# Optimization experiments

Measured on AMD Instinct MI355X. Metric: run time of the kernel, lower is better.

The kernel has to match this reference:

```python
import jax, jax.numpy as jnp
import numpy as np

N = 100000
E = 1600000
F_IN = 64
HID = 64
OUT = 64


def _sage_conv(x, src, dst, w_l, b_l, w_r):
    # PyG SAGEConv (mean aggr): out = lin_l(mean_{j in N(i)} x_j) + lin_r(x_i)
    msgs = x[src]                                             # [E, F] gather
    summed = jax.ops.segment_sum(msgs, dst, num_segments=N)   # [N, F]
    ones = jnp.ones((src.shape[0],), dtype=x.dtype)
    cnt = jax.ops.segment_sum(ones, dst, num_segments=N)      # [N]
    mean = summed / jnp.maximum(cnt, 1.0)[:, None]
    return mean @ w_l + b_l + x @ w_r


def setup_inputs() -> dict:
    key = jax.random.key(0)
    ks = jax.random.split(key, 12)
    sc = lambda f: 1.0 / np.sqrt(f)
    inp = {
        "h": jax.random.normal(ks[0], (N, F_IN), dtype=jnp.float32),
        "edge_index": jax.random.randint(ks[1], (2, E), 0, N, dtype=jnp.int64),
        # conv1: lin_l (with bias) and lin_r (no bias), weights stored [in, out]
        "w1_l": jax.random.normal(ks[2], (F_IN, HID), dtype=jnp.float32) * sc(F_IN),
        "b1_l": jnp.zeros((HID,), dtype=jnp.float32),
        "w1_r": jax.random.normal(ks[3], (F_IN, HID), dtype=jnp.float32) * sc(F_IN),
        "w_lin1": jax.random.normal(ks[4], (HID, HID), dtype=jnp.float32) * sc(HID),
        "b_lin1": jnp.zeros((HID,), dtype=jnp.float32),
        "w2_l": jax.random.normal(ks[5], (HID, HID), dtype=jnp.float32) * sc(HID),
        "b2_l": jnp.zeros((HID,), dtype=jnp.float32),
        "w2_r": jax.random.normal(ks[6], (HID, HID), dtype=jnp.float32) * sc(HID),
        "w_lin2": jax.random.normal(ks[7], (HID, OUT), dtype=jnp.float32) * sc(HID),
        "b_lin2": jnp.zeros((OUT,), dtype=jnp.float32),
    }
    return inp


def reference(h, edge_index, w1_l, b1_l, w1_r, w_lin1, b_lin1,
              w2_l, b2_l, w2_r, w_lin2, b_lin2):
    src, dst = edge_index[0], edge_index[1]
    x = jax.nn.relu(_sage_conv(h, src, dst, w1_l, b1_l, w1_r))
    x = jax.nn.relu(x @ w_lin1 + b_lin1)
    x = jax.nn.relu(_sage_conv(x, src, dst, w2_l, b2_l, w2_r))
    x = x @ w_lin2 + b_lin2
    return x
```

## Files before the change

kernel.cpp:

```cpp
#include <hip/hip_runtime.h>
#include <hip/hip_fp16.h>

#define FEAT   64
#define BSHIFT 8
#define BNODES 256
#define MAXB   512
#define CHUNK  4096
#define REGION 5120

typedef _Float16 half8 __attribute__((ext_vector_type(8)));
typedef float  float4v __attribute__((ext_vector_type(4)));

__global__ __launch_bounds__(512) void prep_kernel(
    const int* __restrict__ esrc, const int* __restrict__ edst,
    int* __restrict__ bcur, int* __restrict__ pedge, int E, int PB,
    const float* __restrict__ h, __half* __restrict__ h16,
    int n4, int CVB,
    const float* w0, const float* w1, const float* w2,
    const float* w3, const float* w4, const float* w5,
    __half* __restrict__ wT)
{
    __shared__ int cnt[MAXB];
    __shared__ int sa[MAXB], sb[MAXB];
    __shared__ int gb[MAXB];
    __shared__ int lcur[MAXB];
    __shared__ int stage[CHUNK];
    __shared__ int tgt[CHUNK];

    int b   = blockIdx.x;
    int tid = threadIdx.x;

    if (b >= PB) {
        int bb = b - PB;
        if (bb < CVB) {
            int i = bb * 512 + tid;
            if (i < n4) {
                float4 v = ((const float4*)h)[i];
                union { uint2 u; __half2 h2[2]; } r;
                r.h2[0] = __floats2half2_rn(v.x, v.y);
                r.h2[1] = __floats2half2_rn(v.z, v.w);
                ((uint2*)h16)[i] = r.u;
            }
        } else {
            int idx = (bb - CVB) * 512 + tid;
            int m = idx >> 12;
            int e = idx & 4095;
            const float* src = m==0?w0 : m==1?w1 : m==2?w2 : m==3?w3 : m==4?w4 : w5;
            int o = e >> 6, i = e & 63;
            wT[m * 4096 + o * 64 + i] = __float2half(src[i * 64 + o]);
        }
        return;
    }

    cnt[tid] = 0;
    __syncthreads();

    int base = b * CHUNK;
    int vals[8];
    int bs[8];
#pragma unroll
    for (int i = 0; i < 8; i++) {
        int e = base + tid + i * 512;
        bs[i] = -1;
        if (e < E) {
            int s_ = esrc[e];
            int d_ = edst[e];
            int bk = d_ >> BSHIFT;
            bs[i]  = bk;
            vals[i] = s_ | ((d_ & (BNODES - 1)) << 20);
            atomicAdd(&cnt[bk], 1);
        }
    }
    __syncthreads();

    sa[tid] = cnt[tid];
    __syncthreads();
    int* cur = sa; int* nxt = sb;
    for (int off = 1; off < MAXB; off <<= 1) {
        nxt[tid] = cur[tid] + ((tid >= off) ? cur[tid - off] : 0);
        __syncthreads();
        int* tmp = cur; cur = nxt; nxt = tmp;
    }
    {
        int c = cnt[tid];
        int lo = cur[tid] - c;
        int gbase = c ? atomicAdd(&bcur[tid], c) : 0;
        if (gbase > REGION) gbase = REGION;
        gb[tid]   = tid * REGION + gbase - lo;
        lcur[tid] = lo;
    }
    __syncthreads();

#pragma unroll
    for (int i = 0; i < 8; i++) {
        if (bs[i] >= 0) {
            int pos = atomicAdd(&lcur[bs[i]], 1);
            stage[pos] = vals[i];
            tgt[pos]   = gb[bs[i]];
        }
    }
    __syncthreads();

    int cn = min(CHUNK, E - base);
    for (int i = tid; i < cn; i += 512)
        pedge[tgt[i] + i] = stage[i];
}

__global__ __launch_bounds__(512) void buildcsr_kernel(
    const int* __restrict__ pedge, const int* __restrict__ bcur,
    unsigned* __restrict__ rowinfo, int* __restrict__ csr, int N)
{
    __shared__ int stg[REGION];
    __shared__ int srt[REGION];
    __shared__ int hist[BNODES], scn[BNODES], lcur[BNODES];
    int b = blockIdx.x;
    int tid = threadIdx.x;
    int beg = b * REGION;
    int cnt = min(bcur[b], REGION);

    if (tid < BNODES) hist[tid] = 0;
    __syncthreads();

    for (int i = tid; i < cnt; i += 512) {
        int p = pedge[beg + i];
        stg[i] = p;
        atomicAdd(&hist[p >> 20], 1);
    }
    __syncthreads();

    int v = 0;
    if (tid < BNODES) { v = hist[tid]; scn[tid] = v; }
    __syncthreads();
    for (int off = 1; off < BNODES; off <<= 1) {
        int t = 0;
        if (tid < BNODES && tid >= off) t = scn[tid - off];
        __syncthreads();
        if (tid < BNODES) scn[tid] += t;
        __syncthreads();
    }
    if (tid < BNODES) {
        int excl = scn[tid] - v;
        int node = (b << BSHIFT) + tid;
        if (node < N)
            rowinfo[node] = (unsigned)(beg + excl) | ((unsigned)v << 21);
        lcur[tid] = excl;
    }
    __syncthreads();

    for (int i = tid; i < cnt; i += 512) {
        int p = stg[i];
        int pos = atomicAdd(&lcur[p >> 20], 1);
        srt[pos] = p & 0xFFFFF;
    }
    __syncthreads();
    for (int i = tid; i < cnt; i += 512)
        csr[beg + i] = srt[i];
}

__global__ __launch_bounds__(256, 4) void fused_layer_kernel(
    const __half* __restrict__ x, const unsigned* __restrict__ rowinfo,
    const int* __restrict__ csr_src,
    const __half* __restrict__ wlT, const __half* __restrict__ wrT,
    const __half* __restrict__ w2T,
    const float* __restrict__ b1, const float* __restrict__ b2,
    float* __restrict__ out_f, __half* __restrict__ out_h,
    int n, int relu_out)
{
    __shared__ __attribute__((aligned(16))) _Float16 sbuf[64][72];

    int tid  = threadIdx.x;
    int wave = tid >> 6;
    int lane = tid & 63;
    int sg   = tid >> 4;
    int gg   = (tid >> 3) & 1;
    int s8   = tid & 7;
    int r    = lane & 15;
    int q    = lane >> 4;
    int base = blockIdx.x * 64 + wave * 16;

    int arow = min(base + r, n - 1);
    const half8* xrow = (const half8*)(x + (size_t)arow * FEAT);
    half8 Ax0 = xrow[q], Ax1 = xrow[4 + q];

    unsigned infos[4];
#pragma unroll
    for (int i = 0; i < 4; i++) {
        int node = blockIdx.x * 64 + sg * 4 + i;
        infos[i] = (node < n) ? rowinfo[node] : 0u;
    }

    int beg4[4], deg4[4];
    int itmax = 0;
#pragma unroll
    for (int i = 0; i < 4; i++) {
        beg4[i] = (int)(infos[i] & 0x1FFFFFu);
        deg4[i] = (int)(infos[i] >> 21);
        int it = (deg4[i] + 3) >> 2;
        itmax = max(itmax, it);
    }
    float acc[4][8];
#pragma unroll
    for (int i = 0; i < 4; i++)
#pragma unroll
        for (int t = 0; t < 8; t++) acc[i][t] = 0.f;

    int  c0[4], c1[4];
    bool p0[4], p1[4];
#pragma unroll
    for (int i = 0; i < 4; i++) {
        int be = beg4[i] + gg;
        int en = beg4[i] + deg4[i];
        p0[i] = be < en;
        p1[i] = be + 2 < en;
        c0[i] = csr_src[p0[i] ? be : beg4[i]];
        c1[i] = csr_src[p1[i] ? be + 2 : beg4[i]];
    }

    for (int it = 0; it < itmax; ++it) {
        int  n0[4], n1[4];
        bool m0[4], m1[4];
#pragma unroll
        for (int i = 0; i < 4; i++) {
            int be = beg4[i] + gg + (it + 1) * 4;
            int en = beg4[i] + deg4[i];
            m0[i] = be < en;
            m1[i] = be + 2 < en;
            n0[i] = csr_src[m0[i] ? be : beg4[i]];
            n1[i] = csr_src[m1[i] ? be + 2 : beg4[i]];
        }
#pragma unroll
        for (int i = 0; i < 4; i++) {
            int j0 = p0[i] ? c0[i] : 0;
            int j1 = p1[i] ? c1[i] : 0;
            union { uint4 u; __half2 h2[4]; } r0, r1;
            r0.u = ((const uint4*)(x + (size_t)j0 * FEAT))[s8];
            r1.u = ((const uint4*)(x + (size_t)j1 * FEAT))[s8];
            float w0 = p0[i] ? 1.0f : 0.0f;
            float w1 = p1[i] ? 1.0f : 0.0f;
#pragma unroll
            for (int t = 0; t < 4; t++) {
                float2 f0 = __half22float2(r0.h2[t]);
                float2 f1 = __half22float2(r1.h2[t]);
                acc[i][2*t]   = fmaf(w0, f0.x, acc[i][2*t]);
                acc[i][2*t]   = fmaf(w1, f1.x, acc[i][2*t]);
                acc[i][2*t+1] = fmaf(w0, f0.y, acc[i][2*t+1]);
                acc[i][2*t+1] = fmaf(w1, f1.y, acc[i][2*t+1]);
            }
        }
#pragma unroll
        for (int i = 0; i < 4; i++) {
            c0[i] = n0[i]; c1[i] = n1[i];
            p0[i] = m0[i]; p1[i] = m1[i];
        }
    }

#pragma unroll
    for (int i = 0; i < 4; i++) {
#pragma unroll
        for (int t = 0; t < 8; t++)
            acc[i][t] += __shfl_xor(acc[i][t], 8, 64);
        if (gg == 0) {
            int deg = deg4[i];
            float inv = deg ? 1.0f / (float)deg : 0.0f;
            union { uint4 u; __half2 h2[4]; } o;
            o.h2[0] = __floats2half2_rn(acc[i][0]*inv, acc[i][1]*inv);
            o.h2[1] = __floats2half2_rn(acc[i][2]*inv, acc[i][3]*inv);
            o.h2[2] = __floats2half2_rn(acc[i][4]*inv, acc[i][5]*inv);
            o.h2[3] = __floats2half2_rn(acc[i][6]*inv, acc[i][7]*inv);
            int ln = sg * 4 + i;
            *(uint4*)&sbuf[ln][s8 * 8] = o.u;
        }
    }
    __syncthreads();

    union { uint4 u4; half8 h; } Am0u, Am1u;
    Am0u.u4 = *(const uint4*)&sbuf[wave * 16 + r][q * 8];
    Am1u.u4 = *(const uint4*)&sbuf[wave * 16 + r][(4 + q) * 8];

    float4v acc1[4];
#pragma unroll
    for (int c = 0; c < 4; c++) {
        float bv = b1[c * 16 + r];
        acc1[c] = (float4v){bv, bv, bv, bv};
        const half8* bl = (const half8*)(wlT + (size_t)(c * 16 + r) * FEAT);
        const half8* br = (const half8*)(wrT + (size_t)(c * 16 + r) * FEAT);
        acc1[c] = __builtin_amdgcn_mfma_f32_16x16x32_f16(Am0u.h, bl[q],     acc1[c], 0, 0, 0);
        acc1[c] = __builtin_amdgcn_mfma_f32_16x16x32_f16(Am1u.h, bl[4 + q], acc1[c], 0, 0, 0);
        acc1[c] = __builtin_amdgcn_mfma_f32_16x16x32_f16(Ax0,    br[q],     acc1[c], 0, 0, 0);
        acc1[c] = __builtin_amdgcn_mfma_f32_16x16x32_f16(Ax1,    br[4 + q], acc1[c], 0, 0, 0);
    }
#pragma unroll
    for (int c = 0; c < 4; c++)
#pragma unroll
        for (int t = 0; t < 4; t++)
            sbuf[wave * 16 + q * 4 + t][c * 16 + r] = (_Float16)fmaxf(acc1[c][t], 0.0f);
    __syncthreads();

    union { uint4 u4; half8 h; } A2[2];
#pragma unroll
    for (int s = 0; s < 2; s++)
        A2[s].u4 = *(const uint4*)&sbuf[wave * 16 + r][s * 32 + q * 8];

    float4v acc2[4];
#pragma unroll
    for (int c = 0; c < 4; c++) {
        float bv = b2[c * 16 + r];
        acc2[c] = (float4v){bv, bv, bv, bv};
        const half8* bw = (const half8*)(w2T + (size_t)(c * 16 + r) * FEAT);
        acc2[c] = __builtin_amdgcn_mfma_f32_16x16x32_f16(A2[0].h, bw[q],     acc2[c], 0, 0, 0);
        acc2[c] = __builtin_amdgcn_mfma_f32_16x16x32_f16(A2[1].h, bw[4 + q], acc2[c], 0, 0, 0);
    }

#pragma unroll
    for (int c = 0; c < 4; c++)
#pragma unroll
        for (int t = 0; t < 4; t++) {
            int gr = base + q * 4 + t;
            if (gr < n) {
                float v = acc2[c][t];
                if (relu_out) v = fmaxf(v, 0.0f);
                if (out_h) out_h[(size_t)gr * FEAT + c * 16 + r] = __float2half(v);
                else       out_f[(size_t)gr * FEAT + c * 16 + r] = v;
            }
        }
}

extern "C" void kernel_launch(void* const* d_in, const int* in_sizes, int n_in,
                              void* d_out, int out_size, void* d_ws, size_t ws_size,
                              hipStream_t stream) {
    const float* h      = (const float*)d_in[0];
    const int*   ei     = (const int*)d_in[1];
    const float* w1_l   = (const float*)d_in[2];
    const float* b1_l   = (const float*)d_in[3];
    const float* w1_r   = (const float*)d_in[4];
    const float* w_lin1 = (const float*)d_in[5];
    const float* b_lin1 = (const float*)d_in[6];
    const float* w2_l   = (const float*)d_in[7];
    const float* b2_l   = (const float*)d_in[8];
    const float* w2_r   = (const float*)d_in[9];
    const float* w_lin2 = (const float*)d_in[10];
    const float* b_lin2 = (const float*)d_in[11];

    const int N = in_sizes[0] / FEAT;
    const int E = in_sizes[1] / 2;
    const int* src  = ei;
    const int* dst_ = ei + E;

    const int NB  = (N + BNODES - 1) >> BSHIFT;
    const int PB  = (E + CHUNK - 1) / CHUNK;
    const int n4  = N * FEAT / 4;
    const int CVB = (n4 + 511) / 512;
    const int fblk = (N + 63) / 64;

    size_t off = 0;
    int* bcur       = (int*)d_ws + off; off += MAXB;
    unsigned* rowinfo = (unsigned*)((int*)d_ws + off); off += (size_t)N;
    off = (off + 3) & ~(size_t)3;
    int* csr    = (int*)d_ws + off; off += (size_t)NB * REGION + 64;
    off = (off + 3) & ~(size_t)3;
    __half* h16 = (__half*)((int*)d_ws + off); off += (size_t)N * FEAT / 2;
    __half* x2h = (__half*)((int*)d_ws + off); off += (size_t)N * FEAT / 2;
    __half* wT  = (__half*)((int*)d_ws + off); off += 6 * 2048;
    int* pedge  = (int*)d_ws + off; off += (size_t)NB * REGION;

    hipMemsetAsync(bcur, 0, MAXB * sizeof(int), stream);
    prep_kernel<<<PB + CVB + 48, 512, 0, stream>>>(
        src, dst_, bcur, pedge, E, PB,
        h, h16, n4, CVB,
        w1_l, w1_r, w_lin1, w2_l, w2_r, w_lin2, wT);
    buildcsr_kernel<<<NB, 512, 0, stream>>>(pedge, bcur, rowinfo, csr, N);

    fused_layer_kernel<<<fblk, 256, 0, stream>>>(
        h16, rowinfo, csr,
        wT + 0 * 4096, wT + 1 * 4096, wT + 2 * 4096,
        b1_l, b_lin1, (float*)nullptr, x2h, N, 1);

    fused_layer_kernel<<<fblk, 256, 0, stream>>>(
        x2h, rowinfo, csr,
        wT + 3 * 4096, wT + 4 * 4096, wT + 5 * 4096,
        b2_l, b_lin2, (float*)d_out, (__half*)nullptr, N, 0);
}
```

Baseline: 235.2 us.

## Halve destination bucket size and edge chunk in CSR build

Shrinks the bucket from 256 to 128 destination nodes, which doubles the bucket count to 1024. Edge chunks per prep block shrink from 4096 to 2048. Each of the 512 threads now scans and allocates two buckets, and the separate count array is merged into the scan buffer. The aim is smaller per-bucket regions in buildcsr, giving more blocks and more parallelism for CSR construction and the fused layers' locality, at the cost of more global atomics on bcur and a longer scan in prep.

```diff
diff --git a/kernel.cpp b/kernel.cpp
--- a/kernel.cpp
+++ b/kernel.cpp
@@ -2,11 +2,11 @@
 #include <hip/hip_fp16.h>
 
 #define FEAT   64
-#define BSHIFT 8
-#define BNODES 256
-#define MAXB   512
-#define CHUNK  4096
-#define REGION 5120
+#define BSHIFT 7
+#define BNODES 128
+#define MAXB   1024
+#define CHUNK  2048
+#define REGION 2560
 
 typedef _Float16 half8 __attribute__((ext_vector_type(8)));
 typedef float  float4v __attribute__((ext_vector_type(4)));
@@ -20,10 +20,8 @@
     const float* w3, const float* w4, const float* w5,
     __half* __restrict__ wT)
 {
-    __shared__ int cnt[MAXB];
     __shared__ int sa[MAXB], sb[MAXB];
-    __shared__ int gb[MAXB];
-    __shared__ int lcur[MAXB];
+    __shared__ int gb[MAXB], lcur[MAXB];
     __shared__ int stage[CHUNK];
     __shared__ int tgt[CHUNK];
 
@@ -52,14 +50,15 @@
         return;
     }
 
-    cnt[tid] = 0;
+    sa[tid] = 0;
+    sa[tid + 512] = 0;
     __syncthreads();
 
     int base = b * CHUNK;
-    int vals[8];
-    int bs[8];
-#pragma unroll
-    for (int i = 0; i < 8; i++) {
+    int vals[4];
+    int bs[4];
+#pragma unroll
+    for (int i = 0; i < 4; i++) {
         int e = base + tid + i * 512;
         bs[i] = -1;
         if (e < E) {
@@ -68,31 +67,40 @@
             int bk = d_ >> BSHIFT;
             bs[i]  = bk;
             vals[i] = s_ | ((d_ & (BNODES - 1)) << 20);
-            atomicAdd(&cnt[bk], 1);
-        }
-    }
-    __syncthreads();
-
-    sa[tid] = cnt[tid];
-    __syncthreads();
+            atomicAdd(&sa[bk], 1);
+        }
+    }
+    __syncthreads();
+
+    int cA = sa[tid];
+    int cB = sa[tid + 512];
+
     int* cur = sa; int* nxt = sb;
     for (int off = 1; off < MAXB; off <<= 1) {
         nxt[tid] = cur[tid] + ((tid >= off) ? cur[tid - off] : 0);
+        int j = tid + 512;
+        nxt[j] = cur[j] + cur[j - off];
         __syncthreads();
         int* tmp = cur; cur = nxt; nxt = tmp;
     }
     {
-        int c = cnt[tid];
-        int lo = cur[tid] - c;
-        int gbase = c ? atomicAdd(&bcur[tid], c) : 0;
-        if (gbase > REGION) gbase = REGION;
-        gb[tid]   = tid * REGION + gbase - lo;
+        int lo = cur[tid] - cA;
+        int g0 = cA ? atomicAdd(&bcur[tid], cA) : 0;
+        if (g0 > REGION) g0 = REGION;
+        gb[tid]   = tid * REGION + g0 - lo;
         lcur[tid] = lo;
-    }
-    __syncthreads();
-
-#pragma unroll
-    for (int i = 0; i < 8; i++) {
+
+        int j  = tid + 512;
+        int lo2 = cur[j] - cB;
+        int g1 = cB ? atomicAdd(&bcur[j], cB) : 0;
+        if (g1 > REGION) g1 = REGION;
+        gb[j]   = j * REGION + g1 - lo2;
+        lcur[j] = lo2;
+    }
+    __syncthreads();
+
+#pragma unroll
+    for (int i = 0; i < 4; i++) {
         if (bs[i] >= 0) {
             int pos = atomicAdd(&lcur[bs[i]], 1);
             stage[pos] = vals[i];
@@ -361,7 +369,7 @@
     __half* h16 = (__half*)((int*)d_ws + off); off += (size_t)N * FEAT / 2;
     __half* x2h = (__half*)((int*)d_ws + off); off += (size_t)N * FEAT / 2;
     __half* wT  = (__half*)((int*)d_ws + off); off += 6 * 2048;
-    int* pedge  = (int*)d_ws + off; off += (size_t)NB * REGION;
+    int* pedge  = (int*)d_ws + off; off += (size_t)NB * REGION + 64;
 
     hipMemsetAsync(bcur, 0, MAXB * sizeof(int), stream);
     prep_kernel<<<PB + CVB + 48, 512, 0, stream>>>(
```

Measured after the change: 246.7 us. 4.9% more time.

## Replace block-local bucket scan with per-edge global atomics on padded counters

Applied to the files above, without the earlier changes.

The edge-bucketing pass no longer builds a shared-memory histogram, prefix scan and staged scatter per chunk. Each edge instead takes its slot with a global atomic on a per-bucket counter, padded to 16 ints to avoid false sharing, and writes straight into its bucket region. The CSR build also drops its shared staging buffer and reads pedge from global memory twice. This removes several block syncs and a large shared-memory footprint, but it issues 1.6M global atomics on only about 400 hot counters, so contention may dominate.

```diff
diff --git a/kernel.cpp b/kernel.cpp
--- a/kernel.cpp
+++ b/kernel.cpp
@@ -7,6 +7,7 @@
 #define MAXB   512
 #define CHUNK  4096
 #define REGION 5120
+#define CPAD   16
 
 typedef _Float16 half8 __attribute__((ext_vector_type(8)));
 typedef float  float4v __attribute__((ext_vector_type(4)));
@@ -20,13 +21,6 @@
     const float* w3, const float* w4, const float* w5,
     __half* __restrict__ wT)
 {
-    __shared__ int cnt[MAXB];
-    __shared__ int sa[MAXB], sb[MAXB];
-    __shared__ int gb[MAXB];
-    __shared__ int lcur[MAXB];
-    __shared__ int stage[CHUNK];
-    __shared__ int tgt[CHUNK];
-
     int b   = blockIdx.x;
     int tid = threadIdx.x;
 
@@ -52,80 +46,37 @@
         return;
     }
 
-    cnt[tid] = 0;
-    __syncthreads();
-
     int base = b * CHUNK;
-    int vals[8];
-    int bs[8];
 #pragma unroll
     for (int i = 0; i < 8; i++) {
         int e = base + tid + i * 512;
-        bs[i] = -1;
         if (e < E) {
             int s_ = esrc[e];
             int d_ = edst[e];
             int bk = d_ >> BSHIFT;
-            bs[i]  = bk;
-            vals[i] = s_ | ((d_ & (BNODES - 1)) << 20);
-            atomicAdd(&cnt[bk], 1);
-        }
-    }
-    __syncthreads();
-
-    sa[tid] = cnt[tid];
-    __syncthreads();
-    int* cur = sa; int* nxt = sb;
-    for (int off = 1; off < MAXB; off <<= 1) {
-        nxt[tid] = cur[tid] + ((tid >= off) ? cur[tid - off] : 0);
-        __syncthreads();
-        int* tmp = cur; cur = nxt; nxt = tmp;
-    }
-    {
-        int c = cnt[tid];
-        int lo = cur[tid] - c;
-        int gbase = c ? atomicAdd(&bcur[tid], c) : 0;
-        if (gbase > REGION) gbase = REGION;
-        gb[tid]   = tid * REGION + gbase - lo;
-        lcur[tid] = lo;
-    }
-    __syncthreads();
-
-#pragma unroll
-    for (int i = 0; i < 8; i++) {
-        if (bs[i] >= 0) {
-            int pos = atomicAdd(&lcur[bs[i]], 1);
-            stage[pos] = vals[i];
-            tgt[pos]   = gb[bs[i]];
-        }
-    }
-    __syncthreads();
-
-    int cn = min(CHUNK, E - base);
-    for (int i = tid; i < cn; i += 512)
-        pedge[tgt[i] + i] = stage[i];
+            int pos = atomicAdd(&bcur[bk * CPAD], 1);
+            if (pos < REGION)
+                pedge[bk * REGION + pos] = s_ | ((d_ & (BNODES - 1)) << 20);
+        }
+    }
 }
 
 __global__ __launch_bounds__(512) void buildcsr_kernel(
     const int* __restrict__ pedge, const int* __restrict__ bcur,
     unsigned* __restrict__ rowinfo, int* __restrict__ csr, int N)
 {
-    __shared__ int stg[REGION];
     __shared__ int srt[REGION];
     __shared__ int hist[BNODES], scn[BNODES], lcur[BNODES];
     int b = blockIdx.x;
     int tid = threadIdx.x;
     int beg = b * REGION;
-    int cnt = min(bcur[b], REGION);
+    int cnt = min(bcur[b * CPAD], REGION);
 
     if (tid < BNODES) hist[tid] = 0;
     __syncthreads();
 
-    for (int i = tid; i < cnt; i += 512) {
-        int p = pedge[beg + i];
-        stg[i] = p;
-        atomicAdd(&hist[p >> 20], 1);
-    }
+    for (int i = tid; i < cnt; i += 512)
+        atomicAdd(&hist[pedge[beg + i] >> 20], 1);
     __syncthreads();
 
     int v = 0;
@@ -148,7 +99,7 @@
     __syncthreads();
 
     for (int i = tid; i < cnt; i += 512) {
-        int p = stg[i];
+        int p = pedge[beg + i];
         int pos = atomicAdd(&lcur[p >> 20], 1);
         srt[pos] = p & 0xFFFFF;
     }
@@ -353,7 +304,7 @@
     const int fblk = (N + 63) / 64;
 
     size_t off = 0;
-    int* bcur       = (int*)d_ws + off; off += MAXB;
+    int* bcur       = (int*)d_ws + off; off += (size_t)MAXB * CPAD;
     unsigned* rowinfo = (unsigned*)((int*)d_ws + off); off += (size_t)N;
     off = (off + 3) & ~(size_t)3;
     int* csr    = (int*)d_ws + off; off += (size_t)NB * REGION + 64;
@@ -361,9 +312,9 @@
     __half* h16 = (__half*)((int*)d_ws + off); off += (size_t)N * FEAT / 2;
     __half* x2h = (__half*)((int*)d_ws + off); off += (size_t)N * FEAT / 2;
     __half* wT  = (__half*)((int*)d_ws + off); off += 6 * 2048;
-    int* pedge  = (int*)d_ws + off; off += (size_t)NB * REGION;
-
-    hipMemsetAsync(bcur, 0, MAXB * sizeof(int), stream);
+    int* pedge  = (int*)d_ws + off; off += (size_t)NB * REGION + 64;
+
+    hipMemsetAsync(bcur, 0, (size_t)MAXB * CPAD * sizeof(int), stream);
     prep_kernel<<<PB + CVB + 48, 512, 0, stream>>>(
         src, dst_, bcur, pedge, E, PB,
         h, h16, n4, CVB,
```

Measured after the change: 299.4 us. +27.3%, slower.
